# Optimization experiments

Hardware: AMD Instinct MI355X
Metric: run time of the kernel (lower is better)

## Reference

```python
import jax, jax.numpy as jnp
import numpy as np

B, S, D = 2, 1024, 2048
H, HKV, HD = 32, 8, 64  # query heads, kv heads, head_dim
REP = H // HKV
ROPE_THETA = 10000.0


def _rope_tables(seq_len, head_dim, theta):
    inv_freq = 1.0 / (theta ** (jnp.arange(0, head_dim, 2, dtype=jnp.float32) / head_dim))
    pos = jnp.arange(seq_len, dtype=jnp.float32)
    freqs = jnp.outer(pos, inv_freq)            # [S, HD/2]
    emb = jnp.concatenate([freqs, freqs], -1)   # [S, HD]
    return jnp.cos(emb), jnp.sin(emb)


def setup_inputs() -> dict:
    key = jax.random.key(0)
    kx, kq, kk, kv, ko = jax.random.split(key, 5)
    scale = 0.02
    x = jax.random.normal(kx, (B, S, D), jnp.float32)
    wq = jax.random.normal(kq, (D, H * HD), jnp.float32) * scale
    wk = jax.random.normal(kk, (D, HKV * HD), jnp.float32) * scale
    wv = jax.random.normal(kv, (D, HKV * HD), jnp.float32) * scale
    wo = jax.random.normal(ko, (H * HD, D), jnp.float32) * scale
    cos, sin = _rope_tables(S, HD, ROPE_THETA)
    return {"x": x, "wq": wq, "wk": wk, "wv": wv, "wo": wo,
            "cos": cos, "sin": sin, "start_pos": 0}


def _rotate_half(t):
    t1, t2 = jnp.split(t, 2, axis=-1)
    return jnp.concatenate([-t2, t1], axis=-1)


def reference(x, wq, wk, wv, wo, cos, sin, start_pos):
    b, s, _ = x.shape
    # QKV projections
    xq = (x @ wq).reshape(b, s, H, HD)
    xk = (x @ wk).reshape(b, s, HKV, HD)
    xv = (x @ wv).reshape(b, s, HKV, HD)
    # RoPE (broadcast cos/sin over batch and heads)
    c = cos[None, :, None, :]
    sn = sin[None, :, None, :]
    xq = xq * c + _rotate_half(xq) * sn
    xk = xk * c + _rotate_half(xk) * sn
    # KV cache write + read: with start_pos=0 prefill, keys/values == xk/xv
    keys, values = xk, xv
    # GQA attention without materializing repeat_kv:
    # q grouped as [b, s, kv_head g, rep r, d]
    qg = xq.reshape(b, s, HKV, REP, HD)
    scale = 1.0 / jnp.sqrt(jnp.asarray(HD, xq.dtype))
    scores = jnp.einsum('bqgrd,bkgd->bgrqk', qg, keys) * scale  # [b,g,r,s,s]
    q_pos = start_pos + jnp.arange(s)
    k_pos = jnp.arange(start_pos + s)
    causal = q_pos[:, None] >= k_pos[None, :]                   # [s, kv_len]
    scores = jnp.where(causal[None, None, None], scores, jnp.asarray(-jnp.inf, scores.dtype))
    attn = jax.nn.softmax(scores, axis=-1)
    out = jnp.einsum('bgrqk,bkgd->bqgrd', attn, values)
    out = out.reshape(b, s, H * HD)
    return out @ wo
```

## Files before the change

kernel.cpp:

```cpp
#include <hip/hip_runtime.h>
#include <cstdint>
#include <cstddef>

#define Bsz   2
#define Sseq  1024
#define Ddim  2048
#define Hq    32
#define Hkv   8
#define HDm   64
#define MROWS (Bsz * Sseq)
#define NQc   (Hq * HDm)
#define NKVc  (Hkv * HDm)

typedef __attribute__((ext_vector_type(8))) _Float16 f16x8;
typedef __attribute__((ext_vector_type(4))) float    f32x4;

__device__ __forceinline__ void gload_lds16(const void* g, void* s) {
    __builtin_amdgcn_global_load_lds(
        (const __attribute__((address_space(1))) void*)g,
        (__attribute__((address_space(3))) void*)s, 16, 0, 0);
}

__global__ __launch_bounds__(256)
void conv_split16(const float* __restrict__ in, _Float16* __restrict__ hi,
                  _Float16* __restrict__ lo)
{
    const int i = blockIdx.x * 256 + threadIdx.x;
    const float4 v0 = reinterpret_cast<const float4*>(in)[i * 2];
    const float4 v1 = reinterpret_cast<const float4*>(in)[i * 2 + 1];
    const float a[8] = {v0.x, v0.y, v0.z, v0.w, v1.x, v1.y, v1.z, v1.w};
    f16x8 h, l;
#pragma unroll
    for (int j = 0; j < 8; ++j) {
        const _Float16 hh = (_Float16)a[j];
        h[j] = hh;
        l[j] = (_Float16)(a[j] - (float)hh);
    }
    *reinterpret_cast<f16x8*>(hi + (size_t)i * 8) = h;
    *reinterpret_cast<f16x8*>(lo + (size_t)i * 8) = l;
}

__global__ __launch_bounds__(256)
void conv_w16t(const float* __restrict__ wq, const float* __restrict__ wk,
               const float* __restrict__ wv, const float* __restrict__ wo,
               _Float16* __restrict__ oq, _Float16* __restrict__ ok,
               _Float16* __restrict__ ov, _Float16* __restrict__ oo)
{
    __shared__ float tile[32][33];
    const int id = blockIdx.x;
    const float* src; _Float16* dst; int C, t;
    if (id < 4096)      { src = wq; dst = oq; C = 2048; t = id; }
    else if (id < 5120) { src = wk; dst = ok; C = 512;  t = id - 4096; }
    else if (id < 6144) { src = wv; dst = ov; C = 512;  t = id - 5120; }
    else                { src = wo; dst = oo; C = 2048; t = id - 6144; }
    const int R = 2048;
    const int ctiles = C >> 5;
    const int c0 = (t % ctiles) * 32, r0 = (t / ctiles) * 32;
    const int tx = threadIdx.x & 31, ty = threadIdx.x >> 5;
#pragma unroll
    for (int p = 0; p < 4; ++p) {
        const int r = ty + p * 8;
        tile[r][tx] = src[(size_t)(r0 + r) * C + c0 + tx];
    }
    __syncthreads();
#pragma unroll
    for (int p = 0; p < 4; ++p) {
        const int cc = ty + p * 8;
        dst[(size_t)(c0 + cc) * R + r0 + tx] = (_Float16)tile[tx][cc];
    }
}

__device__ __forceinline__
void gemm2_loop64(const _Float16* __restrict__ Ahi, const _Float16* __restrict__ Alo,
                  const _Float16* __restrict__ Bt, int Kdim, int row0, int col0,
                  _Float16* sAhi, _Float16* sAlo, _Float16* sB,
                  f32x4 (&acc)[2][4])
{
    const int t    = threadIdx.x;
    const int lane = t & 63;
    const int wid  = t >> 6;
    const int wr   = wid >> 1;
    const int wc   = wid & 1;
    const int fr   = lane & 15;
    const int kc   = (lane >> 4) * 8;
    const int srow = lane >> 2;
    const int scol = (lane & 3) * 8;

    for (int k0 = 0; k0 < Kdim; k0 += 32) {
        __syncthreads();
        {
            const size_t ga = (size_t)(row0 + wid * 16 + srow) * Kdim + k0 + scol;
            gload_lds16(Ahi + ga, (char*)sAhi + wid * 1024);
            gload_lds16(Alo + ga, (char*)sAlo + wid * 1024);
#pragma unroll
            for (int c = 0; c < 2; ++c) {
                const int seg = 2 * wid + c;
                const size_t gb = (size_t)(col0 + seg * 16 + srow) * Kdim + k0 + scol;
                gload_lds16(Bt + gb, (char*)sB + seg * 1024);
            }
        }
        __syncthreads();

        f16x8 ah[2], al[2], bb[4];
        const int ar = wr * 32 + fr;
        const int br = wc * 64 + fr;
#pragma unroll
        for (int m = 0; m < 2; ++m) {
            ah[m] = *reinterpret_cast<const f16x8*>(&sAhi[(ar + m * 16) * 32 + kc]);
            al[m] = *reinterpret_cast<const f16x8*>(&sAlo[(ar + m * 16) * 32 + kc]);
        }
#pragma unroll
        for (int n = 0; n < 4; ++n)
            bb[n] = *reinterpret_cast<const f16x8*>(&sB[(br + n * 16) * 32 + kc]);
#pragma unroll
        for (int m = 0; m < 2; ++m)
#pragma unroll
            for (int n = 0; n < 4; ++n) {
                acc[m][n] = __builtin_amdgcn_mfma_f32_16x16x32_f16(ah[m], bb[n], acc[m][n], 0, 0, 0);
                acc[m][n] = __builtin_amdgcn_mfma_f32_16x16x32_f16(al[m], bb[n], acc[m][n], 0, 0, 0);
            }
    }
}

__global__ __launch_bounds__(256)
void gemm_qkv2(const _Float16* __restrict__ xhi, const _Float16* __restrict__ xlo,
               const _Float16* __restrict__ wqT, const _Float16* __restrict__ wkT,
               const _Float16* __restrict__ wvT,
               const float* __restrict__ cosT, const float* __restrict__ sinT,
               _Float16* __restrict__ qh, _Float16* __restrict__ kh,
               _Float16* __restrict__ vT)
{
    __shared__ _Float16 sAhi[64 * 32];
    __shared__ _Float16 sAlo[64 * 32];
    __shared__ _Float16 sB[128 * 32];

    const int bx   = blockIdx.x;
    const int row0 = blockIdx.y * 64;
    const _Float16* Bt; int col0, mode;
    if (bx < 16)      { Bt = wqT; col0 = bx * 128;        mode = 0; }
    else if (bx < 20) { Bt = wkT; col0 = (bx - 16) * 128; mode = 1; }
    else              { Bt = wvT; col0 = (bx - 20) * 128; mode = 2; }

    f32x4 acc[2][4];
#pragma unroll
    for (int m = 0; m < 2; ++m)
#pragma unroll
        for (int n = 0; n < 4; ++n)
            acc[m][n] = (f32x4){0.f, 0.f, 0.f, 0.f};

    gemm2_loop64(xhi, xlo, Bt, Ddim, row0, col0, sAhi, sAlo, sB, acc);

    const int lane = threadIdx.x & 63;
    const int wid  = threadIdx.x >> 6;
    const int wr   = wid >> 1, wc = wid & 1;
    const int fr   = lane & 15, fq = lane >> 4;

    if (mode == 2) {
        const int gg = (col0 + wc * 64) >> 6;
#pragma unroll
        for (int m = 0; m < 2; ++m)
#pragma unroll
            for (int j = 0; j < 4; ++j) {
                const int row = row0 + wr * 32 + m * 16 + fq * 4 + j;
                const int b = row >> 10, s = row & (Sseq - 1);
#pragma unroll
                for (int n = 0; n < 4; ++n)
                    vT[(((size_t)((b * 8 + gg) * 64 + n * 16 + fr)) << 10) + s] =
                        (_Float16)acc[m][n][j];
            }
    } else {
        _Float16* dst = (mode == 0) ? qh : kh;
        const int ldd = (mode == 0) ? NQc : NKVc;
        const float qs = (mode == 0) ? 0.125f : 1.0f;
        const int colb = col0 + wc * 64;
#pragma unroll
        for (int m = 0; m < 2; ++m)
#pragma unroll
            for (int j = 0; j < 4; ++j) {
                const int row = row0 + wr * 32 + m * 16 + fq * 4 + j;
                const int s   = row & (Sseq - 1);
                const float c0 = cosT[s * HDm + fr],      s0 = sinT[s * HDm + fr];
                const float c1 = cosT[s * HDm + 16 + fr], s1 = sinT[s * HDm + 16 + fr];
                const float o0 = acc[m][0][j], o1 = acc[m][1][j];
                const float o2 = acc[m][2][j], o3 = acc[m][3][j];
                _Float16* bp = dst + (size_t)row * ldd + colb;
                bp[fr]      = (_Float16)((o0 * c0 - o2 * s0) * qs);
                bp[16 + fr] = (_Float16)((o1 * c1 - o3 * s1) * qs);
                bp[32 + fr] = (_Float16)((o2 * c0 + o0 * s0) * qs);
                bp[48 + fr] = (_Float16)((o3 * c1 + o1 * s1) * qs);
            }
    }
}

__global__ __launch_bounds__(256)
void gemm_out2(const _Float16* __restrict__ aohi, const _Float16* __restrict__ aolo,
               const _Float16* __restrict__ woT, float* __restrict__ C)
{
    __shared__ _Float16 sAhi[64 * 32];
    __shared__ _Float16 sAlo[64 * 32];
    __shared__ _Float16 sB[128 * 32];

    const int row0 = blockIdx.y * 64;
    const int col0 = blockIdx.x * 128;

    f32x4 acc[2][4];
#pragma unroll
    for (int m = 0; m < 2; ++m)
#pragma unroll
        for (int n = 0; n < 4; ++n)
            acc[m][n] = (f32x4){0.f, 0.f, 0.f, 0.f};

    gemm2_loop64(aohi, aolo, woT, NQc, row0, col0, sAhi, sAlo, sB, acc);

    const int lane = threadIdx.x & 63;
    const int wid  = threadIdx.x >> 6;
    const int wr   = wid >> 1, wc = wid & 1;
    const int fr   = lane & 15, fq = lane >> 4;
#pragma unroll
    for (int m = 0; m < 2; ++m)
#pragma unroll
        for (int j = 0; j < 4; ++j) {
            float* cp = C + (size_t)(row0 + wr * 32 + m * 16 + fq * 4 + j) * Ddim
                          + col0 + wc * 64 + fr;
#pragma unroll
            for (int n = 0; n < 4; ++n) cp[n * 16] = acc[m][n][j];
        }
}

__global__ __launch_bounds__(256)
void flash_mfma(const _Float16* __restrict__ Qh, const _Float16* __restrict__ Kh,
                const _Float16* __restrict__ Vt,
                _Float16* __restrict__ aohi, _Float16* __restrict__ aolo,
                const int* __restrict__ spp)
{
    __shared__ _Float16 Ks[64 * 64];
    __shared__ _Float16 Vs[64 * 64];
    __shared__ _Float16 Ps[4][16 * 64];

    const int qb = blockIdx.x;
    const int h  = blockIdx.y;
    const int b  = blockIdx.z;
    const int g  = h >> 2;
    const int sp = *spp;
    const int t  = threadIdx.x;
    const int lane = t & 63;
    const int wid  = t >> 6;
    const int fr = lane & 15;
    const int fq = lane >> 4;

    f16x8 qf[2];
    {
        const _Float16* qp = Qh + (size_t)(b * Sseq + qb * 64 + wid * 16 + fr) * NQc + h * HDm;
#pragma unroll
        for (int c = 0; c < 2; ++c)
            qf[c] = *reinterpret_cast<const f16x8*>(qp + c * 32 + fq * 8);
    }

    f32x4 accO[4];
    float m_i[4], l_i[4];
#pragma unroll
    for (int n = 0; n < 4; ++n) accO[n] = (f32x4){0.f, 0.f, 0.f, 0.f};
#pragma unroll
    for (int j = 0; j < 4; ++j) { m_i[j] = -1e30f; l_i[j] = 0.f; }

    const int nkb = min(Sseq >> 6, ((qb * 64 + 63 + sp) >> 6) + 1);

    for (int kb = 0; kb < nkb; ++kb) {
        __syncthreads();
#pragma unroll
        for (int c2 = 0; c2 < 2; ++c2) {
            const int idx = t + c2 * 256;
            const int r  = idx >> 3;
            const int ch = idx & 7;
            const int sw = (ch ^ (r & 7)) << 3;
            const uint4 kv = *reinterpret_cast<const uint4*>(
                Kh + (size_t)(b * Sseq + kb * 64 + r) * NKVc + g * HDm + ch * 8);
            *reinterpret_cast<uint4*>(&Ks[r * 64 + sw]) = kv;
            const uint4 vv = *reinterpret_cast<const uint4*>(
                Vt + ((size_t)(b * Hkv + g) * HDm + r) * Sseq + kb * 64 + ch * 8);
            *reinterpret_cast<uint4*>(&Vs[r * 64 + sw]) = vv;
        }
        __syncthreads();

        f32x4 accS[4];
#pragma unroll
        for (int n = 0; n < 4; ++n) accS[n] = (f32x4){0.f, 0.f, 0.f, 0.f};
#pragma unroll
        for (int n = 0; n < 4; ++n)
#pragma unroll
            for (int c = 0; c < 2; ++c) {
                const int r  = n * 16 + fr;
                const int cc = c * 4 + fq;
                const f16x8 kf = *reinterpret_cast<const f16x8*>(
                    &Ks[r * 64 + ((cc ^ (r & 7)) << 3)]);
                accS[n] = __builtin_amdgcn_mfma_f32_16x16x32_f16(qf[c], kf, accS[n], 0, 0, 0);
            }

        if (kb * 64 + 63 > qb * 64 + sp) {
            const int q0 = sp + qb * 64 + wid * 16 + fq * 4;
            const int k0 = kb * 64 + fr;
#pragma unroll
            for (int n = 0; n < 4; ++n)
#pragma unroll
                for (int j = 0; j < 4; ++j)
                    if (k0 + n * 16 > q0 + j) accS[n][j] = -1e30f;
        }

#pragma unroll
        for (int j = 0; j < 4; ++j) {
            float mx = fmaxf(fmaxf(accS[0][j], accS[1][j]), fmaxf(accS[2][j], accS[3][j]));
#pragma unroll
            for (int msk = 1; msk < 16; msk <<= 1)
                mx = fmaxf(mx, __shfl_xor(mx, msk));
            const float mnew = fmaxf(m_i[j], mx);
            const float corr = __expf(m_i[j] - mnew);
            m_i[j] = mnew;
            float rs = 0.f;
#pragma unroll
            for (int n = 0; n < 4; ++n) {
                const float p = __expf(accS[n][j] - mnew);
                accS[n][j] = p;
                rs += p;
            }
#pragma unroll
            for (int msk = 1; msk < 16; msk <<= 1)
                rs += __shfl_xor(rs, msk);
            l_i[j] = l_i[j] * corr + rs;
#pragma unroll
            for (int n = 0; n < 4; ++n) accO[n][j] *= corr;
            const int prow = fq * 4 + j;
#pragma unroll
            for (int n = 0; n < 4; ++n) {
                const int col = n * 16 + fr;
                Ps[wid][prow * 64 + (((col >> 3) ^ (prow & 7)) << 3) + (col & 7)] =
                    (_Float16)accS[n][j];
            }
        }

        f16x8 pa[2];
#pragma unroll
        for (int c = 0; c < 2; ++c) {
            const int cc = c * 4 + fq;
            pa[c] = *reinterpret_cast<const f16x8*>(
                &Ps[wid][fr * 64 + ((cc ^ (fr & 7)) << 3)]);
        }
#pragma unroll
        for (int n = 0; n < 4; ++n)
#pragma unroll
            for (int c = 0; c < 2; ++c) {
                const int r  = n * 16 + fr;
                const int cc = c * 4 + fq;
                const f16x8 vf = *reinterpret_cast<const f16x8*>(
                    &Vs[r * 64 + ((cc ^ (r & 7)) << 3)]);
                accO[n] = __builtin_amdgcn_mfma_f32_16x16x32_f16(pa[c], vf, accO[n], 0, 0, 0);
            }
    }

#pragma unroll
    for (int j = 0; j < 4; ++j) {
        const float inv = 1.0f / l_i[j];
        const size_t rowg = (size_t)(b * Sseq + qb * 64 + wid * 16 + fq * 4 + j) * NQc;
#pragma unroll
        for (int n = 0; n < 4; ++n) {
            const float o = accO[n][j] * inv;
            const _Float16 hh = (_Float16)o;
            aohi[rowg + h * HDm + n * 16 + fr] = hh;
            aolo[rowg + h * HDm + n * 16 + fr] = (_Float16)(o - (float)hh);
        }
    }
}

extern "C" void kernel_launch(void* const* d_in, const int* in_sizes, int n_in,
                              void* d_out, int out_size, void* d_ws, size_t ws_size,
                              hipStream_t stream)
{
    const float* x    = (const float*)d_in[0];
    const float* wq   = (const float*)d_in[1];
    const float* wk   = (const float*)d_in[2];
    const float* wv   = (const float*)d_in[3];
    const float* wo   = (const float*)d_in[4];
    const float* cosT = (const float*)d_in[5];
    const float* sinT = (const float*)d_in[6];
    const int*   spp  = (const int*)d_in[7];
    float*       out  = (float*)d_out;

    char* w = (char*)d_ws;
    _Float16* wqT16 = (_Float16*)(w);
    _Float16* wkT16 = (_Float16*)(w + (8ull  << 20));
    _Float16* wvT16 = (_Float16*)(w + (10ull << 20));
    _Float16* woT16 = (_Float16*)(w + (12ull << 20));
    _Float16* xhi   = (_Float16*)(w + (20ull << 20));
    _Float16* xlo   = (_Float16*)(w + (28ull << 20));
    _Float16* aohi  = (_Float16*)(w + (20ull << 20));
    _Float16* aolo  = (_Float16*)(w + (28ull << 20));
    _Float16* qh    = (_Float16*)(w + (36ull << 20));
    _Float16* kh    = (_Float16*)(w + (44ull << 20));
    _Float16* vT    = (_Float16*)(w + (46ull << 20));

    conv_split16<<<2048, 256, 0, stream>>>(x, xhi, xlo);
    conv_w16t<<<10240, 256, 0, stream>>>(wq, wk, wv, wo, wqT16, wkT16, wvT16, woT16);

    gemm_qkv2<<<dim3(24, 32), 256, 0, stream>>>(xhi, xlo, wqT16, wkT16, wvT16,
                                                cosT, sinT, qh, kh, vT);

    flash_mfma<<<dim3(Sseq / 64, Hq, Bsz), 256, 0, stream>>>(qh, kh, vT, aohi, aolo, spp);

    gemm_out2<<<dim3(16, 32), 256, 0, stream>>>(aohi, aolo, woT16, out);
}
```

Before: 279.3 us.

## Restructure flash attention: 128-query blocks, transposed S, exp2 softmax, reversed order

The flash attention kernel now handles 128 query rows per block with 512 threads, so each K/V tile loaded into LDS is shared by twice as many queries. The QK^T MFMA is computed transposed, which puts each query row in a single lane and cuts the softmax row reductions to two shuffles. The log2(e) factor is folded into the Q scale in the projection GEMM so exp2f can replace __expf. Blocks are launched heaviest-first to reduce causal load imbalance, at the cost of fewer blocks, more threads per block and extra shuffles to broadcast corrections.

New measurement: 264.8 us. -5.2%, faster.

```diff
diff --git a/kernel.cpp b/kernel.cpp
--- a/kernel.cpp
+++ b/kernel.cpp
@@ -171,7 +171,7 @@
     } else {
         _Float16* dst = (mode == 0) ? qh : kh;
         const int ldd = (mode == 0) ? NQc : NKVc;
-        const float qs = (mode == 0) ? 0.125f : 1.0f;
+        const float qs = (mode == 0) ? 0.125f * 1.4426950408889634f : 1.0f;
         const int colb = col0 + wc * 64;
 #pragma unroll
         for (int m = 0; m < 2; ++m)
@@ -227,7 +227,7 @@
         }
 }
 
-__global__ __launch_bounds__(256)
+__global__ __launch_bounds__(512)
 void flash_mfma(const _Float16* __restrict__ Qh, const _Float16* __restrict__ Kh,
                 const _Float16* __restrict__ Vt,
                 _Float16* __restrict__ aohi, _Float16* __restrict__ aolo,
@@ -235,9 +235,9 @@
 {
     __shared__ _Float16 Ks[64 * 64];
     __shared__ _Float16 Vs[64 * 64];
-    __shared__ _Float16 Ps[4][16 * 64];
-
-    const int qb = blockIdx.x;
+    __shared__ _Float16 Ps[8][16 * 64];
+
+    const int qb = (Sseq / 128 - 1) - blockIdx.x;
     const int h  = blockIdx.y;
     const int b  = blockIdx.z;
     const int g  = h >> 2;
@@ -250,35 +250,33 @@
 
     f16x8 qf[2];
     {
-        const _Float16* qp = Qh + (size_t)(b * Sseq + qb * 64 + wid * 16 + fr) * NQc + h * HDm;
-#pragma unroll
-        for (int c = 0; c < 2; ++c)
-            qf[c] = *reinterpret_cast<const f16x8*>(qp + c * 32 + fq * 8);
+        const _Float16* qp = Qh + (size_t)(b * Sseq + qb * 128 + wid * 16 + fr) * NQc + h * HDm;
+        qf[0] = *reinterpret_cast<const f16x8*>(qp + fq * 8);
+        qf[1] = *reinterpret_cast<const f16x8*>(qp + 32 + fq * 8);
     }
 
     f32x4 accO[4];
-    float m_i[4], l_i[4];
 #pragma unroll
     for (int n = 0; n < 4; ++n) accO[n] = (f32x4){0.f, 0.f, 0.f, 0.f};
-#pragma unroll
-    for (int j = 0; j < 4; ++j) { m_i[j] = -1e30f; l_i[j] = 0.f; }
-
-    const int nkb = min(Sseq >> 6, ((qb * 64 + 63 + sp) >> 6) + 1);
+    float m_i = -1e30f, l_i = 0.f;
+
+    char* const pbase = (char*)Ps[wid] + fr * 128;
+    const int swz = (fr & 7) << 4;
+
+    const int nkb = min(Sseq >> 6, ((qb * 128 + 127 + sp) >> 6) + 1);
 
     for (int kb = 0; kb < nkb; ++kb) {
         __syncthreads();
-#pragma unroll
-        for (int c2 = 0; c2 < 2; ++c2) {
-            const int idx = t + c2 * 256;
-            const int r  = idx >> 3;
-            const int ch = idx & 7;
+        {
+            const int r  = t >> 3;
+            const int ch = t & 7;
             const int sw = (ch ^ (r & 7)) << 3;
-            const uint4 kv = *reinterpret_cast<const uint4*>(
-                Kh + (size_t)(b * Sseq + kb * 64 + r) * NKVc + g * HDm + ch * 8);
-            *reinterpret_cast<uint4*>(&Ks[r * 64 + sw]) = kv;
-            const uint4 vv = *reinterpret_cast<const uint4*>(
-                Vt + ((size_t)(b * Hkv + g) * HDm + r) * Sseq + kb * 64 + ch * 8);
-            *reinterpret_cast<uint4*>(&Vs[r * 64 + sw]) = vv;
+            *reinterpret_cast<uint4*>(&Ks[r * 64 + sw]) =
+                *reinterpret_cast<const uint4*>(
+                    Kh + (size_t)(b * Sseq + kb * 64 + r) * NKVc + g * HDm + ch * 8);
+            *reinterpret_cast<uint4*>(&Vs[r * 64 + sw]) =
+                *reinterpret_cast<const uint4*>(
+                    Vt + ((size_t)(b * Hkv + g) * HDm + r) * Sseq + kb * 64 + ch * 8);
         }
         __syncthreads();
 
@@ -293,57 +291,65 @@
                 const int cc = c * 4 + fq;
                 const f16x8 kf = *reinterpret_cast<const f16x8*>(
                     &Ks[r * 64 + ((cc ^ (r & 7)) << 3)]);
-                accS[n] = __builtin_amdgcn_mfma_f32_16x16x32_f16(qf[c], kf, accS[n], 0, 0, 0);
-            }
-
-        if (kb * 64 + 63 > qb * 64 + sp) {
-            const int q0 = sp + qb * 64 + wid * 16 + fq * 4;
-            const int k0 = kb * 64 + fr;
+                accS[n] = __builtin_amdgcn_mfma_f32_16x16x32_f16(kf, qf[c], accS[n], 0, 0, 0);
+            }
+
+        if (kb * 64 + 63 > qb * 128 + wid * 16 + sp) {
+            const int q0 = sp + qb * 128 + wid * 16 + fr;
+            const int k0 = kb * 64 + fq * 4;
 #pragma unroll
             for (int n = 0; n < 4; ++n)
 #pragma unroll
                 for (int j = 0; j < 4; ++j)
-                    if (k0 + n * 16 > q0 + j) accS[n][j] = -1e30f;
-        }
-
-#pragma unroll
-        for (int j = 0; j < 4; ++j) {
-            float mx = fmaxf(fmaxf(accS[0][j], accS[1][j]), fmaxf(accS[2][j], accS[3][j]));
-#pragma unroll
-            for (int msk = 1; msk < 16; msk <<= 1)
-                mx = fmaxf(mx, __shfl_xor(mx, msk));
-            const float mnew = fmaxf(m_i[j], mx);
-            const float corr = __expf(m_i[j] - mnew);
-            m_i[j] = mnew;
-            float rs = 0.f;
-#pragma unroll
-            for (int n = 0; n < 4; ++n) {
-                const float p = __expf(accS[n][j] - mnew);
+                    if (k0 + n * 16 + j > q0) accS[n][j] = -1e30f;
+        }
+
+        float mx = -1e30f;
+#pragma unroll
+        for (int n = 0; n < 4; ++n)
+#pragma unroll
+            for (int j = 0; j < 4; ++j) mx = fmaxf(mx, accS[n][j]);
+        mx = fmaxf(mx, __shfl_xor(mx, 16));
+        mx = fmaxf(mx, __shfl_xor(mx, 32));
+        const float mnew = fmaxf(m_i, mx);
+        const float corr = exp2f(m_i - mnew);
+        m_i = mnew;
+        float rs = 0.f;
+#pragma unroll
+        for (int n = 0; n < 4; ++n)
+#pragma unroll
+            for (int j = 0; j < 4; ++j) {
+                const float p = exp2f(accS[n][j] - mnew);
                 accS[n][j] = p;
                 rs += p;
             }
-#pragma unroll
-            for (int msk = 1; msk < 16; msk <<= 1)
-                rs += __shfl_xor(rs, msk);
-            l_i[j] = l_i[j] * corr + rs;
-#pragma unroll
-            for (int n = 0; n < 4; ++n) accO[n][j] *= corr;
-            const int prow = fq * 4 + j;
-#pragma unroll
-            for (int n = 0; n < 4; ++n) {
-                const int col = n * 16 + fr;
-                Ps[wid][prow * 64 + (((col >> 3) ^ (prow & 7)) << 3) + (col & 7)] =
-                    (_Float16)accS[n][j];
-            }
-        }
-
+        rs += __shfl_xor(rs, 16);
+        rs += __shfl_xor(rs, 32);
+        l_i = l_i * corr + rs;
+
+        {
+            float cj[4];
+#pragma unroll
+            for (int j = 0; j < 4; ++j)
+                cj[j] = __shfl(corr, (lane & 48) + fq * 4 + j);
+#pragma unroll
+            for (int n = 0; n < 4; ++n)
+#pragma unroll
+                for (int j = 0; j < 4; ++j) accO[n][j] *= cj[j];
+        }
+
+#pragma unroll
+        for (int n = 0; n < 4; ++n) {
+            union { _Float16 hh[4]; uint2 u; } pk;
+#pragma unroll
+            for (int j = 0; j < 4; ++j) pk.hh[j] = (_Float16)accS[n][j];
+            *reinterpret_cast<uint2*>(pbase + ((n * 32 + fq * 8) ^ swz)) = pk.u;
+        }
         f16x8 pa[2];
 #pragma unroll
-        for (int c = 0; c < 2; ++c) {
-            const int cc = c * 4 + fq;
-            pa[c] = *reinterpret_cast<const f16x8*>(
-                &Ps[wid][fr * 64 + ((cc ^ (fr & 7)) << 3)]);
-        }
+        for (int c = 0; c < 2; ++c)
+            pa[c] = *reinterpret_cast<const f16x8*>(pbase + ((c * 64 + fq * 16) ^ swz));
+
 #pragma unroll
         for (int n = 0; n < 4; ++n)
 #pragma unroll
@@ -356,13 +362,17 @@
             }
     }
 
+    const float invl = 1.0f / l_i;
+    float iv[4];
+#pragma unroll
+    for (int j = 0; j < 4; ++j)
+        iv[j] = __shfl(invl, (lane & 48) + fq * 4 + j);
 #pragma unroll
     for (int j = 0; j < 4; ++j) {
-        const float inv = 1.0f / l_i[j];
-        const size_t rowg = (size_t)(b * Sseq + qb * 64 + wid * 16 + fq * 4 + j) * NQc;
+        const size_t rowg = (size_t)(b * Sseq + qb * 128 + wid * 16 + fq * 4 + j) * NQc;
 #pragma unroll
         for (int n = 0; n < 4; ++n) {
-            const float o = accO[n][j] * inv;
+            const float o = accO[n][j] * iv[j];
             const _Float16 hh = (_Float16)o;
             aohi[rowg + h * HDm + n * 16 + fr] = hh;
             aolo[rowg + h * HDm + n * 16 + fr] = (_Float16)(o - (float)hh);
@@ -403,7 +413,7 @@
     gemm_qkv2<<<dim3(24, 32), 256, 0, stream>>>(xhi, xlo, wqT16, wkT16, wvT16,
                                                 cosT, sinT, qh, kh, vT);
 
-    flash_mfma<<<dim3(Sseq / 64, Hq, Bsz), 256, 0, stream>>>(qh, kh, vT, aohi, aolo, spp);
+    flash_mfma<<<dim3(Sseq / 128, Hq, Bsz), 512, 0, stream>>>(qh, kh, vT, aohi, aolo, spp);
 
     gemm_out2<<<dim3(16, 32), 256, 0, stream>>>(aohi, aolo, woT16, out);
 }
```
